# Optimization experiments

Measured on AMD Instinct MI355X. Metric: run time of the kernel, lower is better.

Reference implementation:

```python
import jax, jax.numpy as jnp
import numpy as np

B, L = 64, 2048
G, K, D = 16, 16, 256
N = G * K
STEPS = 32
MAX_NODES = 50
LN_EPS = 1e-5


def _gelu(x):
    return jax.nn.gelu(x, approximate=False)  # torch nn.GELU default = exact erf


def _mlp2(x, w1, b1, w2, b2):
    return _gelu(x @ w1 + b1) @ w2 + b2


def setup_inputs() -> dict:
    key = jax.random.key(0)
    ki = iter(jax.random.split(key, 64))
    def nrm(shape, s=0.02):
        return jax.random.normal(next(ki), shape, dtype=jnp.float32) * s
    inp = {}
    inp['src'] = jax.random.randint(next(ki), (B, L), 0, MAX_NODES)
    inp['rel'] = jax.random.randint(next(ki), (B, L), 0, 2)
    inp['tgt'] = jax.random.randint(next(ki), (B, L), 0, MAX_NODES)
    inp['mask'] = jnp.ones((B, L), dtype=bool)  # unused by forward, kept for signature parity
    inp['qsrc'] = jax.random.randint(next(ki), (B,), 0, MAX_NODES)
    inp['qtgt'] = jax.random.randint(next(ki), (B,), 0, MAX_NODES)
    inp['node_embed'] = nrm((MAX_NODES, D), 1.0)
    inp['rel_embed'] = nrm((2, D), 1.0)
    inp['edge_w1'] = nrm((3 * D, D)); inp['edge_b1'] = jnp.zeros((D,), jnp.float32)
    inp['edge_w2'] = nrm((D, D)); inp['edge_b2'] = jnp.zeros((D,), jnp.float32)
    inp['query_w1'] = nrm((2 * D, D)); inp['query_b1'] = jnp.zeros((D,), jnp.float32)
    inp['query_w2'] = nrm((D, D)); inp['query_b2'] = jnp.zeros((D,), jnp.float32)
    inp['gproj'] = nrm((D, G))
    inp['sproj'] = nrm((D, K))
    inp['msg_w1'] = nrm((D, 2 * D)); inp['msg_b1'] = jnp.zeros((2 * D,), jnp.float32)
    inp['msg_w2'] = nrm((2 * D, D)); inp['msg_b2'] = jnp.zeros((D,), jnp.float32)
    inp['gate_w1'] = nrm((D, D)); inp['gate_b1'] = jnp.zeros((D,), jnp.float32)
    inp['gate_w2'] = nrm((D, 1)); inp['gate_b2'] = jnp.zeros((1,), jnp.float32)
    inp['upd_w1'] = nrm((2 * D, 2 * D)); inp['upd_b1'] = jnp.zeros((2 * D,), jnp.float32)
    inp['upd_w2'] = nrm((2 * D, D)); inp['upd_b2'] = jnp.zeros((D,), jnp.float32)
    inp['ln_w'] = jnp.ones((D,), jnp.float32); inp['ln_b'] = jnp.zeros((D,), jnp.float32)
    inp['S_init'] = nrm((N, D))
    inp['head_w1'] = nrm((2 * D, D)); inp['head_b1'] = jnp.zeros((D,), jnp.float32)
    inp['head_w2'] = nrm((D, 2)); inp['head_b2'] = jnp.zeros((2,), jnp.float32)
    return inp


def _forward(src, rel, tgt, mask, qsrc, qtgt,
             node_embed, rel_embed,
             edge_w1, edge_b1, edge_w2, edge_b2,
             query_w1, query_b1, query_w2, query_b2,
             gproj, sproj,
             msg_w1, msg_b1, msg_w2, msg_b2,
             gate_w1, gate_b1, gate_w2, gate_b2,
             upd_w1, upd_b1, upd_w2, upd_b2,
             ln_w, ln_b, S_init,
             head_w1, head_b1, head_w2, head_b2):
    Bsz = src.shape[0]
    se = node_embed[jnp.clip(src, 0, MAX_NODES - 1)]          # (B, L, D)
    te = node_embed[jnp.clip(tgt, 0, MAX_NODES - 1)]
    re = rel_embed[rel]
    Xe = _mlp2(jnp.concatenate([se, re, te], -1), edge_w1, edge_b1, edge_w2, edge_b2)
    q = _mlp2(jnp.concatenate([node_embed[jnp.clip(qsrc, 0, MAX_NODES - 1)],
                               node_embed[jnp.clip(qtgt, 0, MAX_NODES - 1)]], -1),
              query_w1, query_b1, query_w2, query_b2)
    X = jnp.concatenate([Xe, q[:, None, :]], axis=1)          # (B, L+1, D)

    # Eval-mode hierarchical hard routing; X is constant across steps so the
    # message aggregation is loop-invariant and computed once (identical math).
    msg = _mlp2(X, msg_w1, msg_b1, msg_w2, msg_b2)
    gate = jax.nn.sigmoid(_mlp2(X, gate_w1, gate_b1, gate_w2, gate_b2))
    gated_msg = msg * gate                                    # (B, L+1, D)
    ga = jax.nn.one_hot(jnp.argmax(X @ gproj, axis=-1), G, dtype=X.dtype)  # (B,L+1,G)
    sa = jax.nn.one_hot(jnp.argmax(X @ sproj, axis=-1), K, dtype=X.dtype)  # (B,L+1,K)
    full_assign = (ga[..., :, None] * sa[..., None, :]).reshape(Bsz, X.shape[1], N)
    incoming = jnp.einsum('bln,bld->bnd', full_assign, gated_msg)          # (B, N, D)

    S0 = jnp.broadcast_to(S_init, (Bsz, N, D))

    def step(S, _):
        u = _mlp2(jnp.concatenate([S, incoming], -1), upd_w1, upd_b1, upd_w2, upd_b2)
        S = S + u
        mu = S.mean(-1, keepdims=True)
        var = ((S - mu) ** 2).mean(-1, keepdims=True)
        S = (S - mu) / jnp.sqrt(var + LN_EPS) * ln_w + ln_b
        return S, None

    S, _ = jax.lax.scan(step, S0, None, length=STEPS)
    bi = jnp.arange(Bsz)
    s_src = S[bi, jnp.clip(qsrc, 0, N - 1)]                   # (B, D)
    s_tgt = S[bi, jnp.clip(qtgt, 0, N - 1)]
    logits = _mlp2(jnp.concatenate([s_src, s_tgt], -1), head_w1, head_b1, head_w2, head_b2)
    return logits                                             # (B, 2)


def reference(src, rel, tgt, mask, qsrc, qtgt,
              node_embed, rel_embed,
              edge_w1, edge_b1, edge_w2, edge_b2,
              query_w1, query_b1, query_w2, query_b2,
              gproj, sproj,
              msg_w1, msg_b1, msg_w2, msg_b2,
              gate_w1, gate_b1, gate_w2, gate_b2,
              upd_w1, upd_b1, upd_w2, upd_b2,
              ln_w, ln_b, S_init,
              head_w1, head_b1, head_w2, head_b2):
    return _forward(src, rel, tgt, mask, qsrc, qtgt,
                    node_embed, rel_embed,
                    edge_w1, edge_b1, edge_w2, edge_b2,
                    query_w1, query_b1, query_w2, query_b2,
                    gproj, sproj,
                    msg_w1, msg_b1, msg_w2, msg_b2,
                    gate_w1, gate_b1, gate_w2, gate_b2,
                    upd_w1, upd_b1, upd_w2, upd_b2,
                    ln_w, ln_b, S_init,
                    head_w1, head_b1, head_w2, head_b2)
```

## Files before the change

### kernel.cpp

```cpp
#include <hip/hip_runtime.h>
#include <hip/hip_bf16.h>
#include <math.h>

#define NB     64
#define LL     2048
#define DD     256
#define NNODE  256
#define NSTEPS 32

typedef __hip_bfloat16 bf16;
typedef __attribute__((ext_vector_type(8))) short bf16x8;
typedef __attribute__((ext_vector_type(4))) float f32x4;

__device__ __forceinline__ float geluf(float x){ return 0.5f*x*(1.0f+erff(x*0.70710678118654752440f)); }
__device__ __forceinline__ short f2bs(float x){ bf16 h = __float2bfloat16(x); return __builtin_bit_cast(short, h); }
__device__ __forceinline__ float bs2f(short s){ bf16 h = __builtin_bit_cast(bf16, s); return __bfloat162float(h); }

__device__ __forceinline__ void split8(float4 a, float4 b, bf16x8& hi, bf16x8& lo){
  float av[8] = {a.x,a.y,a.z,a.w,b.x,b.y,b.z,b.w};
  #pragma unroll
  for(int j=0;j<8;j++){
    short h = f2bs(av[j]);
    hi[j] = h;
    lo[j] = f2bs(av[j] - bs2f(h));
  }
}
__device__ __forceinline__ bf16x8 cvt8(float4 a, float4 b){
  float av[8] = {a.x,a.y,a.z,a.w,b.x,b.y,b.z,b.w};
  bf16x8 v;
  #pragma unroll
  for(int j=0;j<8;j++) v[j] = f2bs(av[j]);
  return v;
}

__global__ __launch_bounds__(256) void k_precompute(const float* __restrict__ ne,
    const float* __restrict__ re, const float* __restrict__ ew1, const float* __restrict__ eb1,
    float* __restrict__ P){
  __shared__ float a[256];
  int row = blockIdx.x, j = threadIdx.x;
  const float* vec; const float* W;
  if(row < 50){ vec = ne + row*256; W = ew1; }
  else if(row < 52){ vec = re + (row-50)*256; W = ew1 + 256*256; }
  else { vec = ne + (row-52)*256; W = ew1 + 512*256; }
  a[j] = vec[j];
  __syncthreads();
  float acc = 0.f;
  for(int k=0;k<256;k++) acc += a[k]*W[k*256 + j];
  if(row >= 50 && row < 52) acc += eb1[j];
  P[row*256 + j] = acc;
}

__global__ __launch_bounds__(256) void k_query(const int* __restrict__ qsrc, const int* __restrict__ qtgt,
    const float* __restrict__ ne, const float* __restrict__ qw1, const float* __restrict__ qb1,
    const float* __restrict__ qw2, const float* __restrict__ qb2, float* __restrict__ qv){
  __shared__ float a[512];
  __shared__ float h[256];
  int b = blockIdx.x, j = threadIdx.x;
  int s = min(max(qsrc[b],0),49), t = min(max(qtgt[b],0),49);
  a[j]     = ne[s*256 + j];
  a[256+j] = ne[t*256 + j];
  __syncthreads();
  float acc = qb1[j];
  for(int k=0;k<512;k++) acc += a[k]*qw1[k*256+j];
  h[j] = geluf(acc);
  __syncthreads();
  float acc2 = qb2[j];
  for(int k=0;k<256;k++) acc2 += h[k]*qw2[k*256+j];
  qv[b*256+j] = acc2;
}

__global__ __launch_bounds__(256) void k_wprep(
    const float* __restrict__ uw1, const float* __restrict__ uw2,
    const float* __restrict__ ew2, const float* __restrict__ gw1,
    const float* __restrict__ mw1, const float* __restrict__ mw2,
    bf16* __restrict__ WTa, bf16* __restrict__ WT2,
    bf16* __restrict__ Weh, bf16* __restrict__ Wel, bf16* __restrict__ Wg,
    bf16* __restrict__ Wm1, bf16* __restrict__ Wm2){
  int i = blockIdx.x*256 + threadIdx.x;
  { int n = i >> 8, k = i & 255;  WTa[i] = __float2bfloat16(uw1[k*512 + n]); }
  { int n = i >> 9, k = i & 511;  WT2[i] = __float2bfloat16(uw2[k*256 + n]); }
  { int n = i >> 8, k = i & 255;  Wm1[i] = __float2bfloat16(mw1[k*512 + n]); }
  { int n = i >> 9, k = i & 511;  Wm2[i] = __float2bfloat16(mw2[k*256 + n]); }
  if(i < 65536){
    int n = i >> 8, k = i & 255;
    float v = ew2[k*256 + n];
    bf16 h = __float2bfloat16(v);
    Weh[i] = h;
    Wel[i] = __float2bfloat16(v - __bfloat162float(h));
    Wg[i]  = __float2bfloat16(gw1[k*256 + n]);
  }
}

#define AST 260
#define MST 520
__global__ __launch_bounds__(256,2) void k_edge_mfma(
    const int* __restrict__ src, const int* __restrict__ rel, const int* __restrict__ tgt,
    const float* __restrict__ P,
    const bf16* __restrict__ Weh, const bf16* __restrict__ Wel, const float* __restrict__ eb2,
    const bf16* __restrict__ Wg, const float* __restrict__ gb1,
    const float* __restrict__ gw2, const float* __restrict__ gb2,
    const float* __restrict__ gp, const float* __restrict__ sp,
    const bf16* __restrict__ Wm1, const float* __restrict__ mb1,
    const bf16* __restrict__ Wm2, const float* __restrict__ mb2,
    float* __restrict__ incoming)
{
  __shared__ __align__(16) float Af[32*AST];
  __shared__ __align__(16) float Xf[32*AST];
  __shared__ float pv[32*32];
  __shared__ float redG[32*4];
  __shared__ float gatev[32];
  __shared__ int   nidx[32];
  bf16* Mh = (bf16*)Af;

  int tid = threadIdx.x;
  int w = tid>>6, lane = tid&63, l15 = lane&15, l4 = lane>>4;
  int blk = blockIdx.x, b = blk>>6, r0 = (blk&63)*32;

  {
    int rr = tid&31, kb = (tid>>5)*32;
    int gr = b*LL + r0 + rr;
    int s = min(max(src[gr],0),49), rl = rel[gr]&1, t = min(max(tgt[gr],0),49);
    const float* ps = P + s*256;
    const float* pr = P + (50+rl)*256;
    const float* pt = P + (52+t)*256;
    #pragma unroll
    for(int j=0;j<32;j+=4){
      int k = kb+j;
      float4 vs = *(const float4*)(ps+k), vr = *(const float4*)(pr+k), vt = *(const float4*)(pt+k);
      float4 o;
      o.x = geluf(vs.x+vr.x+vt.x); o.y = geluf(vs.y+vr.y+vt.y);
      o.z = geluf(vs.z+vr.z+vt.z); o.w = geluf(vs.w+vr.w+vt.w);
      *(float4*)&Af[rr*AST + k] = o;
    }
  }
  __syncthreads();

  {
    f32x4 acc[2][4];
    #pragma unroll
    for(int mt=0;mt<2;mt++)
    #pragma unroll
    for(int nt=0;nt<4;nt++) acc[mt][nt] = (f32x4){0.f,0.f,0.f,0.f};
    for(int kc=0;kc<8;kc++){
      int k0 = kc*32 + l4*8;
      bf16x8 ah[2], al[2];
      #pragma unroll
      for(int mt=0;mt<2;mt++){
        const float* p = &Af[(mt*16+l15)*AST + k0];
        split8(*(const float4*)p, *(const float4*)(p+4), ah[mt], al[mt]);
      }
      #pragma unroll
      for(int nt=0;nt<4;nt++){
        int n = w*64 + nt*16 + l15;
        bf16x8 wh = *(const bf16x8*)&Weh[n*256 + k0];
        bf16x8 wl = *(const bf16x8*)&Wel[n*256 + k0];
        #pragma unroll
        for(int mt=0;mt<2;mt++){
          acc[mt][nt] = __builtin_amdgcn_mfma_f32_16x16x32_bf16(ah[mt], wh, acc[mt][nt], 0,0,0);
          acc[mt][nt] = __builtin_amdgcn_mfma_f32_16x16x32_bf16(ah[mt], wl, acc[mt][nt], 0,0,0);
          acc[mt][nt] = __builtin_amdgcn_mfma_f32_16x16x32_bf16(al[mt], wh, acc[mt][nt], 0,0,0);
        }
      }
    }
    #pragma unroll
    for(int nt=0;nt<4;nt++){
      int n = w*64 + nt*16 + l15;
      float bb = eb2[n];
      #pragma unroll
      for(int mt=0;mt<2;mt++)
      #pragma unroll
      for(int reg=0;reg<4;reg++){
        int r = mt*16 + l4*4 + reg;
        Xf[r*AST + n] = acc[mt][nt][reg] + bb;
      }
    }
  }
  __syncthreads();

  {
    f32x4 ag[2][4];
    #pragma unroll
    for(int mt=0;mt<2;mt++)
    #pragma unroll
    for(int nt=0;nt<4;nt++) ag[mt][nt] = (f32x4){0.f,0.f,0.f,0.f};
    for(int kc=0;kc<8;kc++){
      int k0 = kc*32 + l4*8;
      bf16x8 xa[2];
      #pragma unroll
      for(int mt=0;mt<2;mt++){
        const float* p = &Xf[(mt*16+l15)*AST + k0];
        xa[mt] = cvt8(*(const float4*)p, *(const float4*)(p+4));
      }
      #pragma unroll
      for(int nt=0;nt<4;nt++){
        int n = w*64 + nt*16 + l15;
        bf16x8 wv = *(const bf16x8*)&Wg[n*256 + k0];
        #pragma unroll
        for(int mt=0;mt<2;mt++)
          ag[mt][nt] = __builtin_amdgcn_mfma_f32_16x16x32_bf16(xa[mt], wv, ag[mt][nt], 0,0,0);
      }
    }
    float gpart[2][4] = {{0.f,0.f,0.f,0.f},{0.f,0.f,0.f,0.f}};
    #pragma unroll
    for(int nt=0;nt<4;nt++){
      int n = w*64 + nt*16 + l15;
      float gb = gb1[n], gw = gw2[n];
      #pragma unroll
      for(int mt=0;mt<2;mt++)
      #pragma unroll
      for(int reg=0;reg<4;reg++)
        gpart[mt][reg] += geluf(ag[mt][nt][reg] + gb)*gw;
    }
    #pragma unroll
    for(int mt=0;mt<2;mt++)
    #pragma unroll
    for(int reg=0;reg<4;reg++){
      float sv = gpart[mt][reg];
      #pragma unroll
      for(int o=1;o<16;o<<=1) sv += __shfl_xor(sv,o);
      if(l15==0) redG[(mt*16 + l4*4 + reg)*4 + w] = sv;
    }
  }
  {
    int r2 = tid>>3, g = tid&7, c0 = g*4;
    const float* W4 = (c0<16)? (gp + c0) : (sp + (c0-16));
    float4 p = {0.f,0.f,0.f,0.f};
    for(int k=0;k<256;k++){
      float x = Xf[r2*AST + k];
      float4 wv = *(const float4*)(W4 + k*16);
      p.x += x*wv.x; p.y += x*wv.y; p.z += x*wv.z; p.w += x*wv.w;
    }
    pv[r2*32+c0+0]=p.x; pv[r2*32+c0+1]=p.y; pv[r2*32+c0+2]=p.z; pv[r2*32+c0+3]=p.w;
  }
  __syncthreads();
  if(tid < 32){
    float ssum = redG[tid*4+0]+redG[tid*4+1]+redG[tid*4+2]+redG[tid*4+3] + gb2[0];
    gatev[tid] = 1.f/(1.f+expf(-ssum));
    float bg = pv[tid*32+0]; int big = 0;
    #pragma unroll
    for(int j=1;j<16;j++){ float x=pv[tid*32+j]; if(x>bg){bg=x;big=j;} }
    float bs = pv[tid*32+16]; int bis = 0;
    #pragma unroll
    for(int j=1;j<16;j++){ float x=pv[tid*32+16+j]; if(x>bs){bs=x;bis=j;} }
    nidx[tid] = big*16 + bis;
  }
  __syncthreads();

  {
    f32x4 a1[2][8];
    #pragma unroll
    for(int mt=0;mt<2;mt++)
    #pragma unroll
    for(int nt=0;nt<8;nt++) a1[mt][nt] = (f32x4){0.f,0.f,0.f,0.f};
    for(int kc=0;kc<8;kc++){
      int k0 = kc*32 + l4*8;
      bf16x8 xa[2];
      #pragma unroll
      for(int mt=0;mt<2;mt++){
        const float* p = &Xf[(mt*16+l15)*AST + k0];
        xa[mt] = cvt8(*(const float4*)p, *(const float4*)(p+4));
      }
      #pragma unroll
      for(int nt=0;nt<8;nt++){
        int n = w*128 + nt*16 + l15;
        bf16x8 wv = *(const bf16x8*)&Wm1[n*256 + k0];
        #pragma unroll
        for(int mt=0;mt<2;mt++)
          a1[mt][nt] = __builtin_amdgcn_mfma_f32_16x16x32_bf16(xa[mt], wv, a1[mt][nt], 0,0,0);
      }
    }
    __syncthreads();
    #pragma unroll
    for(int nt=0;nt<8;nt++){
      int n = w*128 + nt*16 + l15;
      float mb = mb1[n];
      #pragma unroll
      for(int mt=0;mt<2;mt++)
      #pragma unroll
      for(int reg=0;reg<4;reg++){
        int r = mt*16 + l4*4 + reg;
        Mh[r*MST + n] = __float2bfloat16(geluf(a1[mt][nt][reg] + mb));
      }
    }
  }
  __syncthreads();

  {
    f32x4 a2[2][4];
    #pragma unroll
    for(int mt=0;mt<2;mt++)
    #pragma unroll
    for(int nt=0;nt<4;nt++) a2[mt][nt] = (f32x4){0.f,0.f,0.f,0.f};
    for(int kc=0;kc<16;kc++){
      int k0 = kc*32 + l4*8;
      bf16x8 ha[2];
      #pragma unroll
      for(int mt=0;mt<2;mt++) ha[mt] = *(const bf16x8*)&Mh[(mt*16+l15)*MST + k0];
      #pragma unroll
      for(int nt=0;nt<4;nt++){
        int n = w*64 + nt*16 + l15;
        bf16x8 wv = *(const bf16x8*)&Wm2[n*512 + k0];
        #pragma unroll
        for(int mt=0;mt<2;mt++)
          a2[mt][nt] = __builtin_amdgcn_mfma_f32_16x16x32_bf16(ha[mt], wv, a2[mt][nt], 0,0,0);
      }
    }
    #pragma unroll
    for(int nt=0;nt<4;nt++){
      int col = w*64 + nt*16 + l15;
      float mb = mb2[col];
      #pragma unroll
      for(int mt=0;mt<2;mt++)
      #pragma unroll
      for(int reg=0;reg<4;reg++){
        int r = mt*16 + l4*4 + reg;
        float val = (a2[mt][nt][reg] + mb)*gatev[r];
        atomicAdd(&incoming[((size_t)b*NNODE + nidx[r])*256 + col], val);
      }
    }
  }
}

__global__ __launch_bounds__(256) void k_qrow(const float* __restrict__ qv,
    const float* __restrict__ mw1, const float* __restrict__ mb1,
    const float* __restrict__ mw2, const float* __restrict__ mb2,
    const float* __restrict__ gw1, const float* __restrict__ gb1,
    const float* __restrict__ gw2, const float* __restrict__ gb2,
    const float* __restrict__ gp, const float* __restrict__ sp,
    float* __restrict__ incoming){
  __shared__ float x[256];
  __shared__ float mh[512];
  __shared__ float gh[256];
  __shared__ float pv[32];
  __shared__ float rbuf[4];
  __shared__ float gv;
  __shared__ int nn;
  int b = blockIdx.x, j = threadIdx.x;
  x[j] = qv[b*256+j];
  __syncthreads();
  float a0 = mb1[j], a1 = mb1[256+j], g0 = gb1[j];
  for(int k=0;k<256;k++){
    float xv = x[k];
    a0 += xv*mw1[k*512+j];
    a1 += xv*mw1[k*512+256+j];
    g0 += xv*gw1[k*256+j];
  }
  mh[j] = geluf(a0); mh[256+j] = geluf(a1); gh[j] = geluf(g0);
  if(j < 32){
    float s1 = 0.f;
    const float* wq = (j<16)? gp+j : sp+(j-16);
    for(int k=0;k<256;k++) s1 += x[k]*wq[k*16];
    pv[j] = s1;
  }
  __syncthreads();
  float m0 = mb2[j];
  for(int k=0;k<512;k++) m0 += mh[k]*mw2[k*256+j];
  float part = gh[j]*gw2[j];
  for(int o=32;o>0;o>>=1) part += __shfl_down(part,o);
  if((j&63)==0) rbuf[j>>6] = part;
  __syncthreads();
  if(j==0){
    float s1 = rbuf[0]+rbuf[1]+rbuf[2]+rbuf[3];
    gv = 1.f/(1.f+expf(-(s1 + gb2[0])));
    float bg = pv[0]; int big = 0;
    for(int t2=1;t2<16;t2++){ if(pv[t2]>bg){bg=pv[t2];big=t2;} }
    float bs = pv[16]; int bis = 0;
    for(int t2=1;t2<16;t2++){ if(pv[16+t2]>bs){bs=pv[16+t2];bis=t2;} }
    nn = big*16 + bis;
  }
  __syncthreads();
  atomicAdd(&incoming[((size_t)b*NNODE + nn)*256 + j], m0*gv);
}

__device__ __forceinline__ void fma32_2q(const float* Arow, float w0, float w1, float* acc0, float* acc1){
  const float4* ap = (const float4*)Arow;
  #pragma unroll
  for(int i=0;i<8;i++){
    float4 a = ap[i];
    acc0[i*4+0] += a.x*w0; acc0[i*4+1] += a.y*w0;
    acc0[i*4+2] += a.z*w0; acc0[i*4+3] += a.w*w0;
    acc1[i*4+0] += a.x*w1; acc1[i*4+1] += a.y*w1;
    acc1[i*4+2] += a.z*w1; acc1[i*4+3] += a.w*w1;
  }
}
__global__ __launch_bounds__(256,2) void k_cpre(const float* __restrict__ incoming,
    const float* __restrict__ uw1, const float* __restrict__ ub1, float* __restrict__ Cpre){
  __shared__ float ATl[256*32];
  int blk = blockIdx.x, row0 = blk*32;
  int tid = threadIdx.x, rr = tid&31, kb = (tid>>5)*32;
  const float* ip = incoming + (size_t)(row0+rr)*256;
  #pragma unroll
  for(int j=0;j<32;j+=4){
    float4 v = *(const float4*)(ip+kb+j);
    ATl[(kb+j+0)*32+rr]=v.x; ATl[(kb+j+1)*32+rr]=v.y;
    ATl[(kb+j+2)*32+rr]=v.z; ATl[(kb+j+3)*32+rr]=v.w;
  }
  __syncthreads();
  float acc0[32], acc1[32];
  #pragma unroll
  for(int r=0;r<32;r++){acc0[r]=0.f;acc1[r]=0.f;}
  int c = tid;
  float w0 = uw1[256*512 + c], w1 = uw1[256*512 + 256 + c];
  for(int k=0;k<256;k++){
    float w0n = (k<255)? uw1[(257+k)*512 + c] : 0.f;
    float w1n = (k<255)? uw1[(257+k)*512 + 256 + c] : 0.f;
    fma32_2q(&ATl[k*32], w0, w1, acc0, acc1);
    w0 = w0n; w1 = w1n;
  }
  float b0 = ub1[c], b1 = ub1[256+c];
  #pragma unroll
  for(int r=0;r<32;r++){
    size_t ro = (size_t)(row0+r)*512;
    Cpre[ro+c]     = acc0[r]+b0;
    Cpre[ro+256+c] = acc1[r]+b1;
  }
}

#define SROW 264
#define HROW 520
__global__ __launch_bounds__(256,2) void k_steps(
    const float* __restrict__ Sini, const float* __restrict__ Cpre,
    const bf16* __restrict__ WTa, const bf16* __restrict__ WT2,
    const float* __restrict__ ub2, const float* __restrict__ lnw,
    const float* __restrict__ lnb, float* __restrict__ Sout)
{
  __shared__ __align__(16) bf16 Sbf[32*SROW];
  __shared__ __align__(16) bf16 Hbf[32*HROW];
  __shared__ float redA[32*4], redB[32*4];

  int tid = threadIdx.x;
  int w   = tid >> 6;
  int lane= tid & 63;
  int l15 = lane & 15;
  int l4  = lane >> 4;
  int row0 = blockIdx.x * 32;

  f32x4 Sreg[2][4];
  float ub[4], lw[4], lb[4];
  #pragma unroll
  for(int nt=0;nt<4;nt++){
    int col = w*64 + nt*16 + l15;
    ub[nt] = ub2[col]; lw[nt] = lnw[col]; lb[nt] = lnb[col];
  }
  #pragma unroll
  for(int mt=0;mt<2;mt++)
  #pragma unroll
  for(int nt=0;nt<4;nt++){
    int col = w*64 + nt*16 + l15;
    #pragma unroll
    for(int reg=0;reg<4;reg++){
      int r = mt*16 + l4*4 + reg;
      int node = (row0 + r) & 255;
      float v = Sini[node*256 + col];
      Sreg[mt][nt][reg] = v;
      Sbf[r*SROW + col] = __float2bfloat16(v);
    }
  }
  __syncthreads();

  const float* CpreBlk = Cpre + (size_t)row0*512;

  for(int step=0; step<NSTEPS; step++){
    f32x4 acc1[2][8];
    #pragma unroll
    for(int mt=0;mt<2;mt++)
    #pragma unroll
    for(int nt=0;nt<8;nt++) acc1[mt][nt] = (f32x4){0.f,0.f,0.f,0.f};
    for(int kc=0;kc<8;kc++){
      int k0 = kc*32 + l4*8;
      bf16x8 a0 = *(const bf16x8*)&Sbf[(     l15)*SROW + k0];
      bf16x8 a1 = *(const bf16x8*)&Sbf[(16 + l15)*SROW + k0];
      #pragma unroll
      for(int nt=0;nt<8;nt++){
        int n = w*128 + nt*16 + l15;
        bf16x8 bfr = *(const bf16x8*)&WTa[n*256 + k0];
        acc1[0][nt] = __builtin_amdgcn_mfma_f32_16x16x32_bf16(a0, bfr, acc1[0][nt], 0,0,0);
        acc1[1][nt] = __builtin_amdgcn_mfma_f32_16x16x32_bf16(a1, bfr, acc1[1][nt], 0,0,0);
      }
    }
    #pragma unroll
    for(int mt=0;mt<2;mt++)
    #pragma unroll
    for(int nt=0;nt<8;nt++){
      int n = w*128 + nt*16 + l15;
      #pragma unroll
      for(int reg=0;reg<4;reg++){
        int r = mt*16 + l4*4 + reg;
        float h = geluf(acc1[mt][nt][reg] + CpreBlk[(size_t)r*512 + n]);
        Hbf[r*HROW + n] = __float2bfloat16(h);
      }
    }
    __syncthreads();

    f32x4 acc2[2][4];
    #pragma unroll
    for(int mt=0;mt<2;mt++)
    #pragma unroll
    for(int nt=0;nt<4;nt++) acc2[mt][nt] = (f32x4){0.f,0.f,0.f,0.f};
    for(int kc=0;kc<16;kc++){
      int k0 = kc*32 + l4*8;
      bf16x8 a0 = *(const bf16x8*)&Hbf[(     l15)*HROW + k0];
      bf16x8 a1 = *(const bf16x8*)&Hbf[(16 + l15)*HROW + k0];
      #pragma unroll
      for(int nt=0;nt<4;nt++){
        int n = w*64 + nt*16 + l15;
        bf16x8 bfr = *(const bf16x8*)&WT2[n*512 + k0];
        acc2[0][nt] = __builtin_amdgcn_mfma_f32_16x16x32_bf16(a0, bfr, acc2[0][nt], 0,0,0);
        acc2[1][nt] = __builtin_amdgcn_mfma_f32_16x16x32_bf16(a1, bfr, acc2[1][nt], 0,0,0);
      }
    }
    #pragma unroll
    for(int mt=0;mt<2;mt++)
    #pragma unroll
    for(int nt=0;nt<4;nt++)
    #pragma unroll
    for(int reg=0;reg<4;reg++)
      acc2[mt][nt][reg] = Sreg[mt][nt][reg] + acc2[mt][nt][reg] + ub[nt];

    #pragma unroll
    for(int mt=0;mt<2;mt++)
    #pragma unroll
    for(int reg=0;reg<4;reg++){
      float s1 = 0.f, s2 = 0.f;
      #pragma unroll
      for(int nt=0;nt<4;nt++){ float v = acc2[mt][nt][reg]; s1 += v; s2 += v*v; }
      #pragma unroll
      for(int o=1;o<16;o<<=1){ s1 += __shfl_xor(s1,o); s2 += __shfl_xor(s2,o); }
      if(l15 == 0){
        int r = mt*16 + l4*4 + reg;
        redA[r*4+w] = s1; redB[r*4+w] = s2;
      }
    }
    __syncthreads();

    #pragma unroll
    for(int mt=0;mt<2;mt++)
    #pragma unroll
    for(int reg=0;reg<4;reg++){
      int r = mt*16 + l4*4 + reg;
      float ss = redA[r*4+0]+redA[r*4+1]+redA[r*4+2]+redA[r*4+3];
      float qq = redB[r*4+0]+redB[r*4+1]+redB[r*4+2]+redB[r*4+3];
      float mu = ss*(1.f/256.f);
      float rs = rsqrtf(qq*(1.f/256.f) - mu*mu + 1e-5f);
      #pragma unroll
      for(int nt=0;nt<4;nt++){
        int col = w*64 + nt*16 + l15;
        float sv = (acc2[mt][nt][reg]-mu)*rs*lw[nt] + lb[nt];
        Sreg[mt][nt][reg] = sv;
        Sbf[r*SROW + col] = __float2bfloat16(sv);
      }
    }
    __syncthreads();
  }

  #pragma unroll
  for(int mt=0;mt<2;mt++)
  #pragma unroll
  for(int nt=0;nt<4;nt++){
    int col = w*64 + nt*16 + l15;
    #pragma unroll
    for(int reg=0;reg<4;reg++){
      int r = mt*16 + l4*4 + reg;
      Sout[(size_t)(row0+r)*256 + col] = Sreg[mt][nt][reg];
    }
  }
}

__global__ __launch_bounds__(256) void k_head(const int* __restrict__ qsrc, const int* __restrict__ qtgt,
    const float* __restrict__ S, const float* __restrict__ hw1, const float* __restrict__ hb1,
    const float* __restrict__ hw2, const float* __restrict__ hb2, float* __restrict__ out){
  __shared__ float a[512];
  __shared__ float h[256];
  __shared__ float rbuf[8];
  int b = blockIdx.x, j = threadIdx.x;
  int s = min(max(qsrc[b],0),255), t = min(max(qtgt[b],0),255);
  a[j]     = S[((size_t)b*NNODE + s)*256 + j];
  a[256+j] = S[((size_t)b*NNODE + t)*256 + j];
  __syncthreads();
  float acc = hb1[j];
  for(int k=0;k<512;k++) acc += a[k]*hw1[k*256+j];
  h[j] = geluf(acc);
  __syncthreads();
  float p0 = h[j]*hw2[j*2], p1 = h[j]*hw2[j*2+1];
  for(int o=32;o>0;o>>=1){ p0 += __shfl_down(p0,o); p1 += __shfl_down(p1,o); }
  if((j&63)==0){ rbuf[(j>>6)*2] = p0; rbuf[(j>>6)*2+1] = p1; }
  __syncthreads();
  if(j==0){
    out[b*2+0] = rbuf[0]+rbuf[2]+rbuf[4]+rbuf[6] + hb2[0];
    out[b*2+1] = rbuf[1]+rbuf[3]+rbuf[5]+rbuf[7] + hb2[1];
  }
}

extern "C" void kernel_launch(void* const* d_in, const int* in_sizes, int n_in,
                              void* d_out, int out_size, void* d_ws, size_t ws_size,
                              hipStream_t stream){
  (void)in_sizes; (void)n_in; (void)out_size; (void)ws_size;
  const int*  src  = (const int*)d_in[0];
  const int*  rel  = (const int*)d_in[1];
  const int*  tgt  = (const int*)d_in[2];
  const int*  qsrc = (const int*)d_in[4];
  const int*  qtgt = (const int*)d_in[5];
  const float* ne  = (const float*)d_in[6];
  const float* re  = (const float*)d_in[7];
  const float* ew1 = (const float*)d_in[8];  const float* eb1 = (const float*)d_in[9];
  const float* ew2 = (const float*)d_in[10]; const float* eb2 = (const float*)d_in[11];
  const float* qw1 = (const float*)d_in[12]; const float* qb1 = (const float*)d_in[13];
  const float* qw2 = (const float*)d_in[14]; const float* qb2 = (const float*)d_in[15];
  const float* gp  = (const float*)d_in[16]; const float* sp  = (const float*)d_in[17];
  const float* mw1 = (const float*)d_in[18]; const float* mb1 = (const float*)d_in[19];
  const float* mw2 = (const float*)d_in[20]; const float* mb2 = (const float*)d_in[21];
  const float* gw1 = (const float*)d_in[22]; const float* gb1 = (const float*)d_in[23];
  const float* gw2 = (const float*)d_in[24]; const float* gb2 = (const float*)d_in[25];
  const float* uw1 = (const float*)d_in[26]; const float* ub1 = (const float*)d_in[27];
  const float* uw2 = (const float*)d_in[28]; const float* ub2 = (const float*)d_in[29];
  const float* lnw = (const float*)d_in[30]; const float* lnb = (const float*)d_in[31];
  const float* Sini= (const float*)d_in[32];
  const float* hw1 = (const float*)d_in[33]; const float* hb1 = (const float*)d_in[34];
  const float* hw2 = (const float*)d_in[35]; const float* hb2 = (const float*)d_in[36];

  float* ws = (float*)d_ws;
  float* P        = ws;
  float* qv       = ws + 26112;
  float* incoming = ws + 42496;
  float* Cpre     = ws + 4236800;
  float* Sout     = ws + 12625408;
  bf16*  wb       = (bf16*)(ws + 16819712);
  bf16*  WTa = wb;            bf16* WT2 = wb + 131072;
  bf16*  Weh = wb + 262144;   bf16* Wel = wb + 327680;
  bf16*  Wg  = wb + 393216;
  bf16*  Wm1 = wb + 458752;   bf16* Wm2 = wb + 589824;
  float* out = (float*)d_out;

  hipMemsetAsync(incoming, 0, (size_t)4194304*4, stream);
  k_wprep<<<512,256,0,stream>>>(uw1,uw2,ew2,gw1,mw1,mw2,WTa,WT2,Weh,Wel,Wg,Wm1,Wm2);
  k_precompute<<<102,256,0,stream>>>(ne,re,ew1,eb1,P);
  k_query<<<64,256,0,stream>>>(qsrc,qtgt,ne,qw1,qb1,qw2,qb2,qv);
  k_edge_mfma<<<4096,256,0,stream>>>(src,rel,tgt,P,Weh,Wel,eb2,Wg,gb1,gw2,gb2,gp,sp,Wm1,mb1,Wm2,mb2,incoming);
  k_qrow<<<64,256,0,stream>>>(qv,mw1,mb1,mw2,mb2,gw1,gb1,gw2,gb2,gp,sp,incoming);
  k_cpre<<<512,256,0,stream>>>(incoming,uw1,ub1,Cpre);
  k_steps<<<512,256,0,stream>>>(Sini,Cpre,WTa,WT2,ub2,lnw,lnb,Sout);
  k_head<<<64,256,0,stream>>>(qsrc,qtgt,Sout,hw1,hb1,hw2,hb2,out);
}
```

Before: 3.506 ms.

## Enlarge k_steps row tile to 64 rows with 8 waves to reuse weight fragments

The recurrent update kernel now processes 64 rows per block with 512 threads (8 waves) instead of 32 rows with 4 waves. Each wave now covers 4 M-tiles, so every weight fragment loaded from global memory feeds four MFMAs instead of two, halving the total weight traffic across the grid. The Cpre reads also use nontemporal loads. In exchange, the shared memory per block roughly doubles and each thread holds more accumulator registers, which may limit occupancy, and the grid shrinks to 256 blocks.

```diff
diff --git a/kernel.cpp b/kernel.cpp
--- a/kernel.cpp
+++ b/kernel.cpp
@@ -418,35 +418,35 @@
 
 #define SROW 264
 #define HROW 520
-__global__ __launch_bounds__(256,2) void k_steps(
+__global__ __launch_bounds__(512,2) void k_steps(
     const float* __restrict__ Sini, const float* __restrict__ Cpre,
     const bf16* __restrict__ WTa, const bf16* __restrict__ WT2,
     const float* __restrict__ ub2, const float* __restrict__ lnw,
     const float* __restrict__ lnb, float* __restrict__ Sout)
 {
-  __shared__ __align__(16) bf16 Sbf[32*SROW];
-  __shared__ __align__(16) bf16 Hbf[32*HROW];
-  __shared__ float redA[32*4], redB[32*4];
+  __shared__ __align__(16) bf16 Sbf[64*SROW];
+  __shared__ __align__(16) bf16 Hbf[64*HROW];
+  __shared__ float redA[64*8], redB[64*8];
 
   int tid = threadIdx.x;
   int w   = tid >> 6;
   int lane= tid & 63;
   int l15 = lane & 15;
   int l4  = lane >> 4;
-  int row0 = blockIdx.x * 32;
-
-  f32x4 Sreg[2][4];
-  float ub[4], lw[4], lb[4];
-  #pragma unroll
-  for(int nt=0;nt<4;nt++){
-    int col = w*64 + nt*16 + l15;
+  int row0 = blockIdx.x * 64;
+
+  f32x4 Sreg[4][2];
+  float ub[2], lw[2], lb[2];
+  #pragma unroll
+  for(int nt=0;nt<2;nt++){
+    int col = w*32 + nt*16 + l15;
     ub[nt] = ub2[col]; lw[nt] = lnw[col]; lb[nt] = lnb[col];
   }
   #pragma unroll
-  for(int mt=0;mt<2;mt++)
-  #pragma unroll
-  for(int nt=0;nt<4;nt++){
-    int col = w*64 + nt*16 + l15;
+  for(int mt=0;mt<4;mt++)
+  #pragma unroll
+  for(int nt=0;nt<2;nt++){
+    int col = w*32 + nt*16 + l15;
     #pragma unroll
     for(int reg=0;reg<4;reg++){
       int r = mt*16 + l4*4 + reg;
@@ -461,90 +461,99 @@
   const float* CpreBlk = Cpre + (size_t)row0*512;
 
   for(int step=0; step<NSTEPS; step++){
-    f32x4 acc1[2][8];
-    #pragma unroll
-    for(int mt=0;mt<2;mt++)
-    #pragma unroll
-    for(int nt=0;nt<8;nt++) acc1[mt][nt] = (f32x4){0.f,0.f,0.f,0.f};
+    f32x4 acc1[4][4];
+    #pragma unroll
+    for(int mt=0;mt<4;mt++)
+    #pragma unroll
+    for(int nt=0;nt<4;nt++) acc1[mt][nt] = (f32x4){0.f,0.f,0.f,0.f};
+    const bf16* bp1[4];
+    #pragma unroll
+    for(int nt=0;nt<4;nt++) bp1[nt] = WTa + (size_t)(w*64 + nt*16 + l15)*256;
     for(int kc=0;kc<8;kc++){
       int k0 = kc*32 + l4*8;
-      bf16x8 a0 = *(const bf16x8*)&Sbf[(     l15)*SROW + k0];
-      bf16x8 a1 = *(const bf16x8*)&Sbf[(16 + l15)*SROW + k0];
-      #pragma unroll
-      for(int nt=0;nt<8;nt++){
-        int n = w*128 + nt*16 + l15;
-        bf16x8 bfr = *(const bf16x8*)&WTa[n*256 + k0];
-        acc1[0][nt] = __builtin_amdgcn_mfma_f32_16x16x32_bf16(a0, bfr, acc1[0][nt], 0,0,0);
-        acc1[1][nt] = __builtin_amdgcn_mfma_f32_16x16x32_bf16(a1, bfr, acc1[1][nt], 0,0,0);
-      }
-    }
-    #pragma unroll
-    for(int mt=0;mt<2;mt++)
-    #pragma unroll
-    for(int nt=0;nt<8;nt++){
-      int n = w*128 + nt*16 + l15;
+      bf16x8 a[4];
+      #pragma unroll
+      for(int mt=0;mt<4;mt++) a[mt] = *(const bf16x8*)&Sbf[(mt*16 + l15)*SROW + k0];
+      #pragma unroll
+      for(int nt=0;nt<4;nt++){
+        bf16x8 bfr = *(const bf16x8*)(bp1[nt] + k0);
+        #pragma unroll
+        for(int mt=0;mt<4;mt++)
+          acc1[mt][nt] = __builtin_amdgcn_mfma_f32_16x16x32_bf16(a[mt], bfr, acc1[mt][nt], 0,0,0);
+      }
+    }
+    #pragma unroll
+    for(int nt=0;nt<4;nt++){
+      int n = w*64 + nt*16 + l15;
+      #pragma unroll
+      for(int mt=0;mt<4;mt++)
       #pragma unroll
       for(int reg=0;reg<4;reg++){
         int r = mt*16 + l4*4 + reg;
-        float h = geluf(acc1[mt][nt][reg] + CpreBlk[(size_t)r*512 + n]);
-        Hbf[r*HROW + n] = __float2bfloat16(h);
+        float cp = __builtin_nontemporal_load(&CpreBlk[(size_t)r*512 + n]);
+        Hbf[r*HROW + n] = __float2bfloat16(geluf(acc1[mt][nt][reg] + cp));
       }
     }
     __syncthreads();
 
-    f32x4 acc2[2][4];
-    #pragma unroll
-    for(int mt=0;mt<2;mt++)
-    #pragma unroll
-    for(int nt=0;nt<4;nt++) acc2[mt][nt] = (f32x4){0.f,0.f,0.f,0.f};
+    f32x4 acc2[4][2];
+    #pragma unroll
+    for(int mt=0;mt<4;mt++)
+    #pragma unroll
+    for(int nt=0;nt<2;nt++) acc2[mt][nt] = (f32x4){0.f,0.f,0.f,0.f};
+    const bf16* bp2[2];
+    #pragma unroll
+    for(int nt=0;nt<2;nt++) bp2[nt] = WT2 + (size_t)(w*32 + nt*16 + l15)*512;
     for(int kc=0;kc<16;kc++){
       int k0 = kc*32 + l4*8;
-      bf16x8 a0 = *(const bf16x8*)&Hbf[(     l15)*HROW + k0];
-      bf16x8 a1 = *(const bf16x8*)&Hbf[(16 + l15)*HROW + k0];
-      #pragma unroll
-      for(int nt=0;nt<4;nt++){
-        int n = w*64 + nt*16 + l15;
-        bf16x8 bfr = *(const bf16x8*)&WT2[n*512 + k0];
-        acc2[0][nt] = __builtin_amdgcn_mfma_f32_16x16x32_bf16(a0, bfr, acc2[0][nt], 0,0,0);
-        acc2[1][nt] = __builtin_amdgcn_mfma_f32_16x16x32_bf16(a1, bfr, acc2[1][nt], 0,0,0);
-      }
-    }
-    #pragma unroll
-    for(int mt=0;mt<2;mt++)
-    #pragma unroll
-    for(int nt=0;nt<4;nt++)
+      bf16x8 a[4];
+      #pragma unroll
+      for(int mt=0;mt<4;mt++) a[mt] = *(const bf16x8*)&Hbf[(mt*16 + l15)*HROW + k0];
+      #pragma unroll
+      for(int nt=0;nt<2;nt++){
+        bf16x8 bfr = *(const bf16x8*)(bp2[nt] + k0);
+        #pragma unroll
+        for(int mt=0;mt<4;mt++)
+          acc2[mt][nt] = __builtin_amdgcn_mfma_f32_16x16x32_bf16(a[mt], bfr, acc2[mt][nt], 0,0,0);
+      }
+    }
+    #pragma unroll
+    for(int mt=0;mt<4;mt++)
+    #pragma unroll
+    for(int nt=0;nt<2;nt++)
     #pragma unroll
     for(int reg=0;reg<4;reg++)
       acc2[mt][nt][reg] = Sreg[mt][nt][reg] + acc2[mt][nt][reg] + ub[nt];
 
     #pragma unroll
-    for(int mt=0;mt<2;mt++)
+    for(int mt=0;mt<4;mt++)
     #pragma unroll
     for(int reg=0;reg<4;reg++){
       float s1 = 0.f, s2 = 0.f;
       #pragma unroll
-      for(int nt=0;nt<4;nt++){ float v = acc2[mt][nt][reg]; s1 += v; s2 += v*v; }
+      for(int nt=0;nt<2;nt++){ float v = acc2[mt][nt][reg]; s1 += v; s2 += v*v; }
       #pragma unroll
       for(int o=1;o<16;o<<=1){ s1 += __shfl_xor(s1,o); s2 += __shfl_xor(s2,o); }
       if(l15 == 0){
         int r = mt*16 + l4*4 + reg;
-        redA[r*4+w] = s1; redB[r*4+w] = s2;
+        redA[r*8+w] = s1; redB[r*8+w] = s2;
       }
     }
     __syncthreads();
 
     #pragma unroll
-    for(int mt=0;mt<2;mt++)
+    for(int mt=0;mt<4;mt++)
     #pragma unroll
     for(int reg=0;reg<4;reg++){
       int r = mt*16 + l4*4 + reg;
-      float ss = redA[r*4+0]+redA[r*4+1]+redA[r*4+2]+redA[r*4+3];
-      float qq = redB[r*4+0]+redB[r*4+1]+redB[r*4+2]+redB[r*4+3];
+      float ss = 0.f, qq = 0.f;
+      #pragma unroll
+      for(int i=0;i<8;i++){ ss += redA[r*8+i]; qq += redB[r*8+i]; }
       float mu = ss*(1.f/256.f);
       float rs = rsqrtf(qq*(1.f/256.f) - mu*mu + 1e-5f);
       #pragma unroll
-      for(int nt=0;nt<4;nt++){
-        int col = w*64 + nt*16 + l15;
+      for(int nt=0;nt<2;nt++){
+        int col = w*32 + nt*16 + l15;
         float sv = (acc2[mt][nt][reg]-mu)*rs*lw[nt] + lb[nt];
         Sreg[mt][nt][reg] = sv;
         Sbf[r*SROW + col] = __float2bfloat16(sv);
@@ -554,10 +563,10 @@
   }
 
   #pragma unroll
-  for(int mt=0;mt<2;mt++)
-  #pragma unroll
-  for(int nt=0;nt<4;nt++){
-    int col = w*64 + nt*16 + l15;
+  for(int mt=0;mt<4;mt++)
+  #pragma unroll
+  for(int nt=0;nt<2;nt++){
+    int col = w*32 + nt*16 + l15;
     #pragma unroll
     for(int reg=0;reg<4;reg++){
       int r = mt*16 + l4*4 + reg;
@@ -638,6 +647,6 @@
   k_edge_mfma<<<4096,256,0,stream>>>(src,rel,tgt,P,Weh,Wel,eb2,Wg,gb1,gw2,gb2,gp,sp,Wm1,mb1,Wm2,mb2,incoming);
   k_qrow<<<64,256,0,stream>>>(qv,mw1,mb1,mw2,mb2,gw1,gb1,gw2,gb2,gp,sp,incoming);
   k_cpre<<<512,256,0,stream>>>(incoming,uw1,ub1,Cpre);
-  k_steps<<<512,256,0,stream>>>(Sini,Cpre,WTa,WT2,ub2,lnw,lnb,Sout);
+  k_steps<<<256,512,0,stream>>>(Sini,Cpre,WTa,WT2,ub2,lnw,lnb,Sout);
   k_head<<<64,256,0,stream>>>(qsrc,qtgt,Sout,hw1,hb1,hw2,hb2,out);
 }
```

New measurement: 3.327 ms. 5.1% less time.

## Restructure recurrent step kernel into 128-row 1024-thread blocks with chunked hidden

Applied to the files above, without the earlier changes.

The step kernel now processes 128 rows per block with 16 waves. Each wave owns one 16-column slice, so every weight fragment loaded from global memory is reused across 8 M-tiles instead of 2. The 512-wide hidden layer is computed in two 256-wide chunks to halve its LDS footprint. A new pre-pass converts the constant Cpre term to bf16 in a per-thread swizzled layout so each step reads it with vector loads. The cost is fewer blocks (128 instead of 512), which leaves part of the GPU idle, plus extra barriers per step and an extra kernel launch.

```diff
diff --git a/kernel.cpp b/kernel.cpp
--- a/kernel.cpp
+++ b/kernel.cpp
@@ -416,153 +416,149 @@
   }
 }
 
-#define SROW 264
-#define HROW 520
-__global__ __launch_bounds__(256,2) void k_steps(
-    const float* __restrict__ Sini, const float* __restrict__ Cpre,
+__global__ __launch_bounds__(256) void k_cswz(const float* __restrict__ Cpre, bf16* __restrict__ Cswz){
+  int gid = blockIdx.x*256 + threadIdx.x;
+  int blk = gid >> 10, tid = gid & 1023;
+  int w = tid >> 6, lane = tid & 63, l15 = lane & 15, l4 = lane >> 4;
+  size_t base = (size_t)gid * 64;
+  int row0 = blk * 128;
+  #pragma unroll
+  for(int j=0;j<64;j++){
+    int ch = j >> 5, mt = (j >> 2) & 7, reg = j & 3;
+    int r = mt*16 + l4*4 + reg;
+    int n = ch*256 + w*16 + l15;
+    Cswz[base + j] = __float2bfloat16(Cpre[(size_t)(row0 + r)*512 + n]);
+  }
+}
+
+#define SROW2 264
+#define HCH   264
+__global__ __launch_bounds__(1024,4) void k_steps(
+    const float* __restrict__ Sini, const bf16* __restrict__ Cswz,
     const bf16* __restrict__ WTa, const bf16* __restrict__ WT2,
     const float* __restrict__ ub2, const float* __restrict__ lnw,
     const float* __restrict__ lnb, float* __restrict__ Sout)
 {
-  __shared__ __align__(16) bf16 Sbf[32*SROW];
-  __shared__ __align__(16) bf16 Hbf[32*HROW];
-  __shared__ float redA[32*4], redB[32*4];
+  __shared__ __align__(16) bf16 Sbf[128*SROW2];
+  __shared__ __align__(16) bf16 Hch[128*HCH];
+  __shared__ float redA[128*16], redB[128*16];
 
   int tid = threadIdx.x;
   int w   = tid >> 6;
   int lane= tid & 63;
   int l15 = lane & 15;
   int l4  = lane >> 4;
-  int row0 = blockIdx.x * 32;
-
-  f32x4 Sreg[2][4];
-  float ub[4], lw[4], lb[4];
-  #pragma unroll
-  for(int nt=0;nt<4;nt++){
-    int col = w*64 + nt*16 + l15;
-    ub[nt] = ub2[col]; lw[nt] = lnw[col]; lb[nt] = lnb[col];
-  }
-  #pragma unroll
-  for(int mt=0;mt<2;mt++)
-  #pragma unroll
-  for(int nt=0;nt<4;nt++){
-    int col = w*64 + nt*16 + l15;
-    #pragma unroll
-    for(int reg=0;reg<4;reg++){
-      int r = mt*16 + l4*4 + reg;
-      int node = (row0 + r) & 255;
-      float v = Sini[node*256 + col];
-      Sreg[mt][nt][reg] = v;
-      Sbf[r*SROW + col] = __float2bfloat16(v);
-    }
-  }
-  __syncthreads();
-
-  const float* CpreBlk = Cpre + (size_t)row0*512;
+  int row0 = blockIdx.x * 128;
+  int col  = w*16 + l15;
+
+  float ub = ub2[col], lw = lnw[col], lb = lnb[col];
+
+  f32x4 Sreg[8];
+  #pragma unroll
+  for(int mt=0;mt<8;mt++)
+  #pragma unroll
+  for(int reg=0;reg<4;reg++){
+    int r = mt*16 + l4*4 + reg;
+    int node = (row0 + r) & 255;
+    float v = Sini[node*256 + col];
+    Sreg[mt][reg] = v;
+    Sbf[r*SROW2 + col] = __float2bfloat16(v);
+  }
+  __syncthreads();
+
+  const bf16* cbase = Cswz + ((size_t)blockIdx.x*1024 + tid)*64;
+  const bf16* wp1base = WTa + (size_t)col*256 + l4*8;
+  const bf16* wp2base = WT2 + (size_t)col*512 + l4*8;
 
   for(int step=0; step<NSTEPS; step++){
-    f32x4 acc1[2][8];
-    #pragma unroll
-    for(int mt=0;mt<2;mt++)
-    #pragma unroll
-    for(int nt=0;nt<8;nt++) acc1[mt][nt] = (f32x4){0.f,0.f,0.f,0.f};
-    for(int kc=0;kc<8;kc++){
-      int k0 = kc*32 + l4*8;
-      bf16x8 a0 = *(const bf16x8*)&Sbf[(     l15)*SROW + k0];
-      bf16x8 a1 = *(const bf16x8*)&Sbf[(16 + l15)*SROW + k0];
-      #pragma unroll
-      for(int nt=0;nt<8;nt++){
-        int n = w*128 + nt*16 + l15;
-        bf16x8 bfr = *(const bf16x8*)&WTa[n*256 + k0];
-        acc1[0][nt] = __builtin_amdgcn_mfma_f32_16x16x32_bf16(a0, bfr, acc1[0][nt], 0,0,0);
-        acc1[1][nt] = __builtin_amdgcn_mfma_f32_16x16x32_bf16(a1, bfr, acc1[1][nt], 0,0,0);
-      }
-    }
-    #pragma unroll
-    for(int mt=0;mt<2;mt++)
-    #pragma unroll
-    for(int nt=0;nt<8;nt++){
-      int n = w*128 + nt*16 + l15;
+    f32x4 acc2[8];
+    #pragma unroll
+    for(int mt=0;mt<8;mt++) acc2[mt] = (f32x4){0.f,0.f,0.f,0.f};
+
+    #pragma unroll
+    for(int ch=0; ch<2; ch++){
+      f32x4 acc1[8];
+      #pragma unroll
+      for(int mt=0;mt<8;mt++) acc1[mt] = (f32x4){0.f,0.f,0.f,0.f};
+      const bf16* wp1 = wp1base + (size_t)ch*256*256;
+      for(int kc=0;kc<8;kc++){
+        int k0 = kc*32 + l4*8;
+        bf16x8 bfr = *(const bf16x8*)(wp1 + kc*32);
+        #pragma unroll
+        for(int mt=0;mt<8;mt++){
+          bf16x8 a = *(const bf16x8*)&Sbf[(mt*16 + l15)*SROW2 + k0];
+          acc1[mt] = __builtin_amdgcn_mfma_f32_16x16x32_bf16(a, bfr, acc1[mt], 0,0,0);
+        }
+      }
+      bf16x8 cf[4];
+      #pragma unroll
+      for(int i=0;i<4;i++) cf[i] = *(const bf16x8*)(cbase + ch*32 + i*8);
+      __syncthreads();
+      #pragma unroll
+      for(int mt=0;mt<8;mt++)
       #pragma unroll
       for(int reg=0;reg<4;reg++){
         int r = mt*16 + l4*4 + reg;
-        float h = geluf(acc1[mt][nt][reg] + CpreBlk[(size_t)r*512 + n]);
-        Hbf[r*HROW + n] = __float2bfloat16(h);
-      }
-    }
-    __syncthreads();
-
-    f32x4 acc2[2][4];
-    #pragma unroll
-    for(int mt=0;mt<2;mt++)
-    #pragma unroll
-    for(int nt=0;nt<4;nt++) acc2[mt][nt] = (f32x4){0.f,0.f,0.f,0.f};
-    for(int kc=0;kc<16;kc++){
-      int k0 = kc*32 + l4*8;
-      bf16x8 a0 = *(const bf16x8*)&Hbf[(     l15)*HROW + k0];
-      bf16x8 a1 = *(const bf16x8*)&Hbf[(16 + l15)*HROW + k0];
-      #pragma unroll
-      for(int nt=0;nt<4;nt++){
-        int n = w*64 + nt*16 + l15;
-        bf16x8 bfr = *(const bf16x8*)&WT2[n*512 + k0];
-        acc2[0][nt] = __builtin_amdgcn_mfma_f32_16x16x32_bf16(a0, bfr, acc2[0][nt], 0,0,0);
-        acc2[1][nt] = __builtin_amdgcn_mfma_f32_16x16x32_bf16(a1, bfr, acc2[1][nt], 0,0,0);
-      }
-    }
-    #pragma unroll
-    for(int mt=0;mt<2;mt++)
-    #pragma unroll
-    for(int nt=0;nt<4;nt++)
+        float c = bs2f(cf[mt>>1][(mt&1)*4 + reg]);
+        Hch[r*HCH + col] = __float2bfloat16(geluf(acc1[mt][reg] + c));
+      }
+      __syncthreads();
+      const bf16* wp2 = wp2base + ch*256;
+      for(int kc=0;kc<8;kc++){
+        int k0 = kc*32 + l4*8;
+        bf16x8 bfr = *(const bf16x8*)(wp2 + kc*32);
+        #pragma unroll
+        for(int mt=0;mt<8;mt++){
+          bf16x8 a = *(const bf16x8*)&Hch[(mt*16 + l15)*HCH + k0];
+          acc2[mt] = __builtin_amdgcn_mfma_f32_16x16x32_bf16(a, bfr, acc2[mt], 0,0,0);
+        }
+      }
+    }
+
+    #pragma unroll
+    for(int mt=0;mt<8;mt++)
     #pragma unroll
     for(int reg=0;reg<4;reg++)
-      acc2[mt][nt][reg] = Sreg[mt][nt][reg] + acc2[mt][nt][reg] + ub[nt];
-
-    #pragma unroll
-    for(int mt=0;mt<2;mt++)
+      acc2[mt][reg] = Sreg[mt][reg] + acc2[mt][reg] + ub;
+
+    #pragma unroll
+    for(int mt=0;mt<8;mt++)
     #pragma unroll
     for(int reg=0;reg<4;reg++){
-      float s1 = 0.f, s2 = 0.f;
-      #pragma unroll
-      for(int nt=0;nt<4;nt++){ float v = acc2[mt][nt][reg]; s1 += v; s2 += v*v; }
+      float v = acc2[mt][reg];
+      float s1 = v, s2 = v*v;
       #pragma unroll
       for(int o=1;o<16;o<<=1){ s1 += __shfl_xor(s1,o); s2 += __shfl_xor(s2,o); }
       if(l15 == 0){
         int r = mt*16 + l4*4 + reg;
-        redA[r*4+w] = s1; redB[r*4+w] = s2;
+        redA[r*16 + w] = s1; redB[r*16 + w] = s2;
       }
     }
     __syncthreads();
 
     #pragma unroll
-    for(int mt=0;mt<2;mt++)
+    for(int mt=0;mt<8;mt++)
     #pragma unroll
     for(int reg=0;reg<4;reg++){
       int r = mt*16 + l4*4 + reg;
-      float ss = redA[r*4+0]+redA[r*4+1]+redA[r*4+2]+redA[r*4+3];
-      float qq = redB[r*4+0]+redB[r*4+1]+redB[r*4+2]+redB[r*4+3];
+      float ss = 0.f, qq = 0.f;
+      #pragma unroll
+      for(int i=0;i<16;i++){ ss += redA[r*16+i]; qq += redB[r*16+i]; }
       float mu = ss*(1.f/256.f);
       float rs = rsqrtf(qq*(1.f/256.f) - mu*mu + 1e-5f);
-      #pragma unroll
-      for(int nt=0;nt<4;nt++){
-        int col = w*64 + nt*16 + l15;
-        float sv = (acc2[mt][nt][reg]-mu)*rs*lw[nt] + lb[nt];
-        Sreg[mt][nt][reg] = sv;
-        Sbf[r*SROW + col] = __float2bfloat16(sv);
-      }
+      float sv = (acc2[mt][reg]-mu)*rs*lw + lb;
+      Sreg[mt][reg] = sv;
+      Sbf[r*SROW2 + col] = __float2bfloat16(sv);
     }
     __syncthreads();
   }
 
   #pragma unroll
-  for(int mt=0;mt<2;mt++)
-  #pragma unroll
-  for(int nt=0;nt<4;nt++){
-    int col = w*64 + nt*16 + l15;
-    #pragma unroll
-    for(int reg=0;reg<4;reg++){
-      int r = mt*16 + l4*4 + reg;
-      Sout[(size_t)(row0+r)*256 + col] = Sreg[mt][nt][reg];
-    }
+  for(int mt=0;mt<8;mt++)
+  #pragma unroll
+  for(int reg=0;reg<4;reg++){
+    int r = mt*16 + l4*4 + reg;
+    Sout[(size_t)(row0+r)*256 + col] = Sreg[mt][reg];
   }
 }
 
@@ -629,6 +625,7 @@
   bf16*  Weh = wb + 262144;   bf16* Wel = wb + 327680;
   bf16*  Wg  = wb + 393216;
   bf16*  Wm1 = wb + 458752;   bf16* Wm2 = wb + 589824;
+  bf16*  Cswz = (bf16*)(ws + 17245696);
   float* out = (float*)d_out;
 
   hipMemsetAsync(incoming, 0, (size_t)4194304*4, stream);
@@ -638,6 +635,7 @@
   k_edge_mfma<<<4096,256,0,stream>>>(src,rel,tgt,P,Weh,Wel,eb2,Wg,gb1,gw2,gb2,gp,sp,Wm1,mb1,Wm2,mb2,incoming);
   k_qrow<<<64,256,0,stream>>>(qv,mw1,mb1,mw2,mb2,gw1,gb1,gw2,gb2,gp,sp,incoming);
   k_cpre<<<512,256,0,stream>>>(incoming,uw1,ub1,Cpre);
-  k_steps<<<512,256,0,stream>>>(Sini,Cpre,WTa,WT2,ub2,lnw,lnb,Sout);
+  k_cswz<<<512,256,0,stream>>>(Cpre,Cswz);
+  k_steps<<<128,1024,0,stream>>>(Sini,Cswz,WTa,WT2,ub2,lnw,lnb,Sout);
   k_head<<<64,256,0,stream>>>(qsrc,qtgt,Sout,hw1,hb1,hw2,hb2,out);
 }
```

After: 4.995 ms. +42.5%, slower.
